# Optimization experiments

Measured on AMD Instinct MI355X. Metric: run time of the kernel, lower is better.

Reference implementation:

```python
import jax, jax.numpy as jnp
import numpy as np

PROP_TIME = 16


def _shift_patches(x):
    """Emulate F.unfold(x, 3, padding=1) for x of shape (B,1,H,W).

    Returns (B, 9, H, W) where channel (ki*3+kj) is x shifted so that
    patches[:, ki*3+kj, h, w] = x_padded[h+ki, w+kj] (row-major 3x3 order,
    matching torch unfold's channel ordering).
    """
    B, _, H, W = x.shape
    xp = jnp.pad(x[:, 0], ((0, 0), (1, 1), (1, 1)))  # (B, H+2, W+2)
    return jnp.stack(
        [xp[:, i:i + H, j:j + W] for i in range(3) for j in range(3)], axis=1
    )  # (B, 9, H, W)


def setup_inputs() -> dict:
    key = jax.random.key(0)
    kg, kx, kd, km = jax.random.split(key, 4)
    B, H, W = 8, 480, 640
    guided = jax.random.normal(kg, (B, 9, H, W), dtype=jnp.float32)
    x = jax.random.normal(kx, (B, 1, H, W), dtype=jnp.float32)
    # so sign() yields a {0,1} validity mask as the module assumes.
    depth = jax.random.uniform(kd, (B, 1, H, W), dtype=jnp.float32) * 10.0
    valid = (jax.random.uniform(km, (B, 1, H, W)) < 0.05).astype(jnp.float32)
    sparse_depth = depth * valid
    return {"guided": guided, "x": x, "sparse_depth": sparse_depth}


def reference(guided, x, sparse_depth):
    # kernel: softmax over the 9 affinity weights per pixel
    kernel = jax.nn.softmax(guided, axis=1)  # (B, 9, H, W)
    sparse_mask = jnp.sign(sparse_depth)      # (B, 1, H, W), {0,1}
    no_sparse_mask = 1.0 - sparse_mask
    x0 = x

    def step(xc, _):
        patches = _shift_patches(xc)                         # (B, 9, H, W)
        out = jnp.sum(patches * kernel, axis=1, keepdims=True)  # (B, 1, H, W)
        out = sparse_mask * x0 + no_sparse_mask * out
        return out, None

    xf, _ = jax.lax.scan(step, x, None, length=PROP_TIME)
    return xf
```

## Files before the change

### kernel.cpp

```cpp
#include <hip/hip_runtime.h>
#include <hip/hip_fp16.h>
#include <math.h>

#define BATCH 8
#define H 480
#define W 640
#define HW (H * W)

#define PS 16
#define PTX 96
#define PTY 128
#define PRX 128
#define PRY 160
#define NT 1024
#define RPT 10
#define NSTRIP 16
#define NBX 7
#define NBY 4
#define NBLK (NBX * NBY * BATCH)
#define NXCD 8
#define BPX (NBLK / NXCD)

typedef __half2 h2;

__device__ __forceinline__ unsigned h2u(h2 v) { return __builtin_bit_cast(unsigned, v); }
__device__ __forceinline__ h2 u2h(unsigned u) { return __builtin_bit_cast(h2, u); }

__device__ __forceinline__ h2 dppLh(h2 v) {
    return u2h((unsigned)__builtin_amdgcn_update_dpp(
        0, (int)h2u(v), 0x138, 0xF, 0xF, false));
}
__device__ __forceinline__ h2 dppRh(h2 v) {
    return u2h((unsigned)__builtin_amdgcn_update_dpp(
        0, (int)h2u(v), 0x130, 0xF, 0xF, false));
}
__device__ __forceinline__ h2 algn(h2 a, h2 b) {
    return u2h(__builtin_amdgcn_alignbit(h2u(a), h2u(b), 16));
}

struct Win { h2 L, C, R; };
__device__ __forceinline__ Win mkwin(h2 c) {
    Win w;
    w.C = c;
    w.L = algn(c, dppLh(c));
    w.R = algn(dppRh(c), c);
    return w;
}

__device__ __forceinline__ h2 rowpx(const h2* wt, h2 bias, Win T, Win M, Win B) {
    h2 a = bias;
    a = __hfma2(wt[0], T.L, a);
    a = __hfma2(wt[1], T.C, a);
    a = __hfma2(wt[2], T.R, a);
    a = __hfma2(wt[3], M.L, a);
    a = __hfma2(wt[4], M.C, a);
    a = __hfma2(wt[5], M.R, a);
    a = __hfma2(wt[6], B.L, a);
    a = __hfma2(wt[7], B.C, a);
    a = __hfma2(wt[8], B.R, a);
    return a;
}

__global__ __launch_bounds__(NT) void prop16_kernel(
    const float* __restrict__ guided,
    const float* __restrict__ x,
    const float* __restrict__ sparse,
    float* __restrict__ xout)
{
    __shared__ unsigned bnd[2][NSTRIP][2][64];

    const int tid  = threadIdx.x;
    const int lane = tid & 63;
    const int strip = tid >> 6;
    const int r0 = strip * RPT;

    const int slot = blockIdx.x;
    const int lb = (slot & (NXCD - 1)) * BPX + (slot >> 3);
    const int b  = lb / (NBX * NBY);
    const int rem = lb - b * (NBX * NBY);
    const int by = rem / NBX;
    const int bx = rem - by * NBX;

    const int bx0 = bx * PTX, by0 = by * PTY;
    const int gx0 = bx0 - PS, gy0 = by0 - PS;
    const size_t ob = (size_t)b * HW;
    const int gx = gx0 + 2 * lane;
    const bool cok = (gx >= 0) && (gx < W);

    h2 xr[RPT];
    h2 wt[RPT][9];
    h2 bs[RPT];
#pragma unroll
    for (int i = 0; i < RPT; ++i) {
        const int gy = gy0 + r0 + i;
        if (cok && gy >= 0 && gy < H) {
            const size_t p = (size_t)gy * W + gx;
            const float2 xf = *(const float2*)(x + ob + p);
            xr[i] = __floats2half2_rn(xf.x, xf.y);
            float2 g[9];
            float se = 0.f, so = 0.f;
#pragma unroll
            for (int k = 0; k < 9; ++k) {
                g[k] = *(const float2*)(guided + ((size_t)(b * 9 + k)) * HW + p);
                g[k].x = __expf(g[k].x); se += g[k].x;
                g[k].y = __expf(g[k].y); so += g[k].y;
            }
            const float2 sv = *(const float2*)(sparse + ob + p);
            const float maske = (sv.x > 0.f) ? 1.f : 0.f;
            const float masko = (sv.y > 0.f) ? 1.f : 0.f;
            const float sce = (1.f - maske) * __builtin_amdgcn_rcpf(se);
            const float sco = (1.f - masko) * __builtin_amdgcn_rcpf(so);
#pragma unroll
            for (int k = 0; k < 9; ++k)
                wt[i][k] = __floats2half2_rn(g[k].x * sce, g[k].y * sco);
            bs[i] = __floats2half2_rn(maske * xf.x, masko * xf.y);
        } else {
            xr[i] = __floats2half2_rn(0.f, 0.f);
#pragma unroll
            for (int k = 0; k < 9; ++k) wt[i][k] = __floats2half2_rn(0.f, 0.f);
            bs[i] = __floats2half2_rn(0.f, 0.f);
        }
    }
    bnd[0][strip][0][lane] = h2u(xr[0]);
    bnd[0][strip][1][lane] = h2u(xr[RPT - 1]);
    __syncthreads();

    for (int t = 0; t < PS; ++t) {
        const int cur = t & 1, nxt = cur ^ 1;
        h2 tp, bp;
        if (strip > 0) tp = u2h(bnd[cur][strip - 1][1][lane]);
        else           tp = xr[0];
        if (strip < NSTRIP - 1) bp = u2h(bnd[cur][strip + 1][0][lane]);
        else                    bp = xr[RPT - 1];
        Win T = mkwin(tp);
        Win M = mkwin(xr[0]);
        h2 nfirst;
#pragma unroll
        for (int r = 0; r < RPT; ++r) {
            const Win B = mkwin((r < RPT - 1) ? xr[r + 1] : bp);
            const h2 n = rowpx(wt[r], bs[r], T, M, B);
            if (r == 0) nfirst = n;
            xr[r] = n;
            T = M; M = B;
        }
        bnd[nxt][strip][0][lane] = h2u(nfirst);
        bnd[nxt][strip][1][lane] = h2u(xr[RPT - 1]);
        __syncthreads();
    }

    if ((2 * lane) >= PS && (2 * lane) < PS + PTX && gx < W) {
#pragma unroll
        for (int i = 0; i < RPT; ++i) {
            const int rr = r0 + i;
            const int gy = gy0 + rr;
            if (rr >= PS && rr < PS + PTY && gy < H) {
                const float2 o = __half22float2(xr[i]);
                *(float2*)(xout + ob + (size_t)gy * W + gx) = o;
            }
        }
    }
}

extern "C" void kernel_launch(void* const* d_in, const int* in_sizes, int n_in,
                              void* d_out, int out_size, void* d_ws, size_t ws_size,
                              hipStream_t stream) {
    const float* guided = (const float*)d_in[0];
    const float* x      = (const float*)d_in[1];
    const float* sparse = (const float*)d_in[2];
    float* out = (float*)d_out;

    dim3 blk(NT, 1, 1);
    dim3 grd(NBLK, 1, 1);
    prop16_kernel<<<grd, blk, 0, stream>>>(guided, x, sparse, out);
}
```

Before: 52.56 us.

## Stage guided affinity loads through LDS with async double-buffered global_load_lds

The prologue now streams the nine guided planes into shared memory with `global_load_lds` in 18 chunks of five rows each, double-buffered per strip. Each chunk is waited on with explicit vmcnt counters, so exp computation on one chunk overlaps the next chunk's fetch. Softmax normalization is deferred: unnormalized exponentials are stored as half2 and later multiplied by a half2 scale that already folds in the sparse mask. This is meant to hide global load latency in the bandwidth-heavy weight-loading phase and cut register pressure from holding all nine float2 loads per row. The cost is extra LDS traffic and hand-managed wait counts, and a small precision risk from storing raw exponentials in half.

```diff
diff --git a/kernel.cpp b/kernel.cpp
--- a/kernel.cpp
+++ b/kernel.cpp
@@ -21,10 +21,20 @@
 #define NXCD 8
 #define BPX (NBLK / NXCD)
 
+#define DEPTH 2
+#define RPC 5
+#define CHUNKS 18
+
 typedef __half2 h2;
 
 __device__ __forceinline__ unsigned h2u(h2 v) { return __builtin_bit_cast(unsigned, v); }
 __device__ __forceinline__ h2 u2h(unsigned u) { return __builtin_bit_cast(h2, u); }
+
+__device__ __forceinline__ void gld_lds(const float* g, float* l) {
+    __builtin_amdgcn_global_load_lds(
+        (const __attribute__((address_space(1))) void*)g,
+        (__attribute__((address_space(3))) void*)l, 4, 0, 0);
+}
 
 __device__ __forceinline__ h2 dppLh(h2 v) {
     return u2h((unsigned)__builtin_amdgcn_update_dpp(
@@ -67,6 +77,7 @@
     const float* __restrict__ sparse,
     float* __restrict__ xout)
 {
+    __shared__ float stg[DEPTH][NSTRIP][RPC][PRX];
     __shared__ unsigned bnd[2][NSTRIP][2][64];
 
     const int tid  = threadIdx.x;
@@ -87,42 +98,80 @@
     const int gx = gx0 + 2 * lane;
     const bool cok = (gx >= 0) && (gx < W);
 
-    h2 xr[RPT];
-    h2 wt[RPT][9];
-    h2 bs[RPT];
+    const int cx0 = min(max(gx0, 0), W - PRX);
+    const int dx  = gx0 - cx0;
+    const float* gpl = guided + (size_t)b * 9 * HW + cx0;
+
+    h2 xr[RPT], bs[RPT];
+    float mke[RPT], mko[RPT], se[RPT], so[RPT];
 #pragma unroll
     for (int i = 0; i < RPT; ++i) {
         const int gy = gy0 + r0 + i;
+        se[i] = 0.f; so[i] = 0.f;
         if (cok && gy >= 0 && gy < H) {
-            const size_t p = (size_t)gy * W + gx;
-            const float2 xf = *(const float2*)(x + ob + p);
+            const size_t p = ob + (size_t)gy * W + gx;
+            const float2 xf = *(const float2*)(x + p);
+            const float2 sv = *(const float2*)(sparse + p);
+            const float me = (sv.x > 0.f) ? 1.f : 0.f;
+            const float mo = (sv.y > 0.f) ? 1.f : 0.f;
             xr[i] = __floats2half2_rn(xf.x, xf.y);
-            float2 g[9];
-            float se = 0.f, so = 0.f;
-#pragma unroll
-            for (int k = 0; k < 9; ++k) {
-                g[k] = *(const float2*)(guided + ((size_t)(b * 9 + k)) * HW + p);
-                g[k].x = __expf(g[k].x); se += g[k].x;
-                g[k].y = __expf(g[k].y); so += g[k].y;
-            }
-            const float2 sv = *(const float2*)(sparse + ob + p);
-            const float maske = (sv.x > 0.f) ? 1.f : 0.f;
-            const float masko = (sv.y > 0.f) ? 1.f : 0.f;
-            const float sce = (1.f - maske) * __builtin_amdgcn_rcpf(se);
-            const float sco = (1.f - masko) * __builtin_amdgcn_rcpf(so);
-#pragma unroll
-            for (int k = 0; k < 9; ++k)
-                wt[i][k] = __floats2half2_rn(g[k].x * sce, g[k].y * sco);
-            bs[i] = __floats2half2_rn(maske * xf.x, masko * xf.y);
+            bs[i] = __floats2half2_rn(me * xf.x, mo * xf.y);
+            mke[i] = 1.f - me; mko[i] = 1.f - mo;
         } else {
             xr[i] = __floats2half2_rn(0.f, 0.f);
-#pragma unroll
-            for (int k = 0; k < 9; ++k) wt[i][k] = __floats2half2_rn(0.f, 0.f);
-            bs[i] = __floats2half2_rn(0.f, 0.f);
+            bs[i] = xr[i];
+            mke[i] = 0.f; mko[i] = 0.f;
         }
     }
     bnd[0][strip][0][lane] = h2u(xr[0]);
     bnd[0][strip][1][lane] = h2u(xr[RPT - 1]);
+
+    asm volatile("s_waitcnt vmcnt(0)" ::: "memory");
+
+    h2 wt[RPT][9];
+#define ISSUE(c_) do {                                                       \
+        const int k_ = (c_) >> 1, pb_ = ((c_) & 1) * RPC;                    \
+        float* lb_ = &stg[(c_) % DEPTH][strip][0][0];                        \
+        _Pragma("unroll")                                                    \
+        for (int rr_ = 0; rr_ < RPC; ++rr_) {                                \
+            const int gy_ = min(max(gy0 + r0 + pb_ + rr_, 0), H - 1);        \
+            const float* gs_ = gpl + (size_t)k_ * HW + (size_t)gy_ * W;      \
+            gld_lds(gs_ + lane,      lb_ + rr_ * PRX);                       \
+            gld_lds(gs_ + 64 + lane, lb_ + rr_ * PRX + 64);                  \
+        }                                                                    \
+    } while (0)
+
+    ISSUE(0);
+    ISSUE(1);
+    int ci = 2 * lane + dx;
+    ci = min(max(ci, 0), PRX - 2);
+#pragma unroll
+    for (int c = 0; c < CHUNKS; ++c) {
+        if (c < CHUNKS - 1) asm volatile("s_waitcnt vmcnt(10)" ::: "memory");
+        else                asm volatile("s_waitcnt vmcnt(0)" ::: "memory");
+        const int k = c >> 1, pb = (c & 1) * RPC;
+        const float* lbc = &stg[c % DEPTH][strip][0][0];
+#pragma unroll
+        for (int rr = 0; rr < RPC; ++rr) {
+            const float2 gv = *(const float2*)(lbc + rr * PRX + ci);
+            const int i = pb + rr;
+            const float ee = __expf(gv.x);
+            const float eo = __expf(gv.y);
+            se[i] += ee; so[i] += eo;
+            wt[i][k] = __floats2half2_rn(ee, eo);
+        }
+        if (c + DEPTH < CHUNKS) ISSUE(c + DEPTH);
+    }
+#undef ISSUE
+
+#pragma unroll
+    for (int i = 0; i < RPT; ++i) {
+        const float sce = mke[i] * __builtin_amdgcn_rcpf(se[i]);
+        const float sco = mko[i] * __builtin_amdgcn_rcpf(so[i]);
+        const h2 sc = __floats2half2_rn(sce, sco);
+#pragma unroll
+        for (int k = 0; k < 9; ++k) wt[i][k] = __hmul2(wt[i][k], sc);
+    }
     __syncthreads();
 
     for (int t = 0; t < PS; ++t) {
```

Measured after the change: 62.78 us. +19.4%, slower.
